# Performance work log

Measured on AMD Instinct MI355X. Metric: run time of the kernel, lower is better.

The kernel has to match this reference:

```python
import jax, jax.numpy as jnp
import numpy as np

N, E = 50000, 800000
IN, HID, OUT = 128, 128, 64
BN_EPS = 1e-5


def setup_inputs() -> dict:
    key = jax.random.key(0)
    ks = jax.random.split(key, 12)
    def glorot(k, shape):
        lim = float(np.sqrt(6.0 / (shape[0] + shape[1])))
        return jax.random.uniform(k, shape, jnp.float32, -lim, lim)
    return {
        "x": jax.random.normal(ks[0], (N, IN), jnp.float32),
        "edge_index": jax.random.randint(ks[1], (2, E), 0, N, jnp.int64),
        "W1": glorot(ks[2], (IN, HID)),  "b1": jnp.zeros((HID,), jnp.float32),
        "W2": glorot(ks[3], (HID, HID)), "b2": jnp.zeros((HID,), jnp.float32),
        "W3": glorot(ks[4], (HID, OUT)), "b3": jnp.zeros((OUT,), jnp.float32),
        "gamma1": jax.random.uniform(ks[5], (HID,), jnp.float32, 0.5, 1.5),
        "beta1": jax.random.normal(ks[6], (HID,), jnp.float32) * 0.1,
        "gamma2": jax.random.uniform(ks[7], (HID,), jnp.float32, 0.5, 1.5),
        "beta2": jax.random.normal(ks[8], (HID,), jnp.float32) * 0.1,
    }


def reference(x, edge_index, W1, b1, W2, b2, W3, b3, gamma1, beta1, gamma2, beta2):
    n = x.shape[0]
    loop = jnp.arange(n, dtype=edge_index.dtype)
    src = jnp.concatenate([edge_index[0], loop])  # add self-loops (PyG GCNConv)
    dst = jnp.concatenate([edge_index[1], loop])
    deg = jax.ops.segment_sum(jnp.ones_like(dst, dtype=x.dtype), dst, num_segments=n)
    dinv = jnp.where(deg > 0, deg ** -0.5, 0.0)
    norm = (dinv[src] * dinv[dst])[:, None]  # symmetric normalization per edge

    def conv(h, W, b):
        h = h @ W                                   # [N, out]
        agg = jax.ops.segment_sum(h[src] * norm, dst, num_segments=n)
        return agg + b

    def bn(h, g, b):  # training-mode BatchNorm1d (batch stats, biased var)
        m = h.mean(axis=0)
        v = h.var(axis=0)
        return (h - m) * jax.lax.rsqrt(v + BN_EPS) * g + b

    # layer 1: in==hidden so residual applies; dropout is a no-op in eval mode
    h = jax.nn.relu(bn(conv(x, W1, b1), gamma1, beta1))
    if h.shape == x.shape:
        h = h + x
    x = h
    # layer 2: hidden -> hidden, residual
    h = jax.nn.relu(bn(conv(x, W2, b2), gamma2, beta2))
    h = h + x
    x = h
    # output layer
    return conv(x, W3, b3)
```

## Files before the change

### kernel.cpp

```cpp
#include <hip/hip_runtime.h>


#define BN_EPS 1e-5f

typedef __attribute__((ext_vector_type(8))) short bf16x8;
typedef __attribute__((ext_vector_type(4))) float f32x4;

__device__ __forceinline__ float bf2f(unsigned short u) {
    unsigned v = ((unsigned)u) << 16;
    return __builtin_bit_cast(float, v);
}
__device__ __forceinline__ unsigned short f2bf(float f) {
    unsigned u = __builtin_bit_cast(unsigned, f);
    u += 0x7fffu + ((u >> 16) & 1u);
    return (unsigned short)(u >> 16);
}

__global__ __launch_bounds__(256) void k_hist_coarse(const int* __restrict__ dst,
                                                     int* __restrict__ ccnt, int e) {
    __shared__ int hist[256];
    const int t = threadIdx.x;
    hist[t] = 0;
    __syncthreads();
    const int base = blockIdx.x * 4096;
    const int end = min(base + 4096, e);
    for (int idx = base + t; idx < end; idx += 256)
        atomicAdd(&hist[dst[idx] >> 8], 1);
    __syncthreads();
    if (hist[t] > 0) atomicAdd(&ccnt[t], hist[t]);
}

__global__ void k_scan_coarse(const int* __restrict__ ccnt, int* __restrict__ cbase,
                              int* __restrict__ ccur) {
    __shared__ int buf[256];
    const int t = threadIdx.x;
    const int v = ccnt[t];
    buf[t] = v;
    __syncthreads();
    for (int off = 1; off < 256; off <<= 1) {
        int add = (t >= off) ? buf[t - off] : 0;
        __syncthreads();
        buf[t] += add;
        __syncthreads();
    }
    const int ex = buf[t] - v;
    cbase[t] = ex;
    ccur[t] = ex;
    if (t == 255) cbase[256] = buf[255];
}

__global__ __launch_bounds__(256) void k_partition(const int* __restrict__ src,
                                                   const int* __restrict__ dst,
                                                   int* __restrict__ ccur,
                                                   unsigned int* __restrict__ pairs, int e) {
    __shared__ unsigned short dl[4096], sl[4096];
    __shared__ int hist[256], basel[256], rnk[256];
    const int t = threadIdx.x;
    const int base = blockIdx.x * 4096;
    hist[t] = 0; rnk[t] = 0;
    __syncthreads();
#pragma unroll
    for (int i = 0; i < 16; ++i) {
        int idx = base + t + i * 256;
        if (idx < e) {
            int d = dst[idx];
            dl[t + i * 256] = (unsigned short)d;
            sl[t + i * 256] = (unsigned short)src[idx];
            atomicAdd(&hist[d >> 8], 1);
        }
    }
    __syncthreads();
    if (hist[t] > 0) basel[t] = atomicAdd(&ccur[t], hist[t]);
    __syncthreads();
#pragma unroll
    for (int i = 0; i < 16; ++i) {
        int idx = base + t + i * 256;
        if (idx < e) {
            int d = dl[t + i * 256];
            int bb = d >> 8;
            int r = atomicAdd(&rnk[bb], 1);
            pairs[basel[bb] + r] = (unsigned)d | ((unsigned)sl[t + i * 256] << 16);
        }
    }
}

__global__ __launch_bounds__(256) void k_fine(const unsigned int* __restrict__ pairs,
                                              const int* __restrict__ cbase,
                                              int* __restrict__ rs, int* __restrict__ eb,
                                              float* __restrict__ dinv, int n, int e) {
    __shared__ int hist[256], fbase[256], cur[256], tmp[256];
    const int t = threadIdx.x;
    const int b = blockIdx.x;
    const int lo = cbase[b], hi = cbase[b + 1];
    hist[t] = 0; cur[t] = 0;
    __syncthreads();
    for (int pos = lo + t; pos < hi; pos += 256)
        atomicAdd(&hist[pairs[pos] & 255], 1);
    __syncthreads();
    const int v = hist[t];
    tmp[t] = v;
    __syncthreads();
    for (int off = 1; off < 256; off <<= 1) {
        int add = (t >= off) ? tmp[t - off] : 0;
        __syncthreads();
        tmp[t] += add;
        __syncthreads();
    }
    fbase[t] = tmp[t] - v;
    __syncthreads();
    const int node = b * 256 + t;
    if (node < n) {
        rs[node] = lo + fbase[t];
        dinv[node] = rsqrtf((float)(hist[t] + 1));
    }
    if (b == 0 && t == 0) rs[n] = e;
    for (int pos = lo + t; pos < hi; pos += 256) {
        unsigned pr = pairs[pos];
        int local = pr & 255;
        int r = atomicAdd(&cur[local], 1);
        eb[lo + fbase[local] + r] = (int)(pr >> 16);
    }
}

__global__ void k_packW(const float* __restrict__ W, unsigned short* __restrict__ Wp, int ncol) {
    const int nct = ncol >> 4;
    int tid = blockIdx.x * 256 + threadIdx.x;
    if (tid >= 4 * nct * 64) return;
    int lane = tid & 63;
    int f = tid >> 6;
    int ct = f % nct;
    int kc = f / nct;
    int n = ct * 16 + (lane & 15);
    int k0 = kc * 32 + (lane >> 4) * 8;
    ushort4 lo, hi;
    lo.x = f2bf(W[(size_t)(k0 + 0) * ncol + n]);
    lo.y = f2bf(W[(size_t)(k0 + 1) * ncol + n]);
    lo.z = f2bf(W[(size_t)(k0 + 2) * ncol + n]);
    lo.w = f2bf(W[(size_t)(k0 + 3) * ncol + n]);
    hi.x = f2bf(W[(size_t)(k0 + 4) * ncol + n]);
    hi.y = f2bf(W[(size_t)(k0 + 5) * ncol + n]);
    hi.z = f2bf(W[(size_t)(k0 + 6) * ncol + n]);
    hi.w = f2bf(W[(size_t)(k0 + 7) * ncol + n]);
    *(ushort4*)(Wp + (size_t)tid * 8)     = lo;
    *(ushort4*)(Wp + (size_t)tid * 8 + 4) = hi;
}

__global__ __launch_bounds__(256) void k_gemm_mfma128(
        const unsigned short* __restrict__ Ab, const unsigned short* __restrict__ Wp,
        unsigned short* __restrict__ xs, const float* __restrict__ dinv, int n) {
    __shared__ __align__(16) unsigned short Wl[16384];
    const int t = threadIdx.x;
    {
        const ushort4* s = (const ushort4*)Wp;
        ushort4* d = (ushort4*)Wl;
#pragma unroll
        for (int i = 0; i < 16; ++i) d[t + 256 * i] = s[t + 256 * i];
    }
    __syncthreads();
    const int lane = t & 63, wave = t >> 6;
    const int quad = lane >> 4, l15 = lane & 15;
    const int m0 = blockIdx.x * 64 + wave * 16;
    const int arow = min(m0 + l15, n - 1);

    f32x4 acc[8];
#pragma unroll
    for (int ct = 0; ct < 8; ++ct) acc[ct] = (f32x4){0.f, 0.f, 0.f, 0.f};

#pragma unroll
    for (int kc = 0; kc < 4; ++kc) {
        bf16x8 a = *(const bf16x8*)(Ab + (size_t)arow * 128 + kc * 32 + quad * 8);
#pragma unroll
        for (int ct = 0; ct < 8; ++ct) {
            bf16x8 b = *(const bf16x8*)(Wl + ((kc * 8 + ct) * 64 + lane) * 8);
            acc[ct] = __builtin_amdgcn_mfma_f32_16x16x32_bf16(a, b, acc[ct], 0, 0, 0);
        }
    }

    int rowv[4]; float dvv[4];
#pragma unroll
    for (int r = 0; r < 4; ++r) {
        rowv[r] = m0 + quad * 4 + r;
        dvv[r] = dinv[min(rowv[r], n - 1)];
    }
#pragma unroll
    for (int ct = 0; ct < 8; ++ct)
#pragma unroll
        for (int r = 0; r < 4; ++r)
            if (rowv[r] < n)
                xs[(size_t)rowv[r] * 128 + ct * 16 + l15] = f2bf(acc[ct][r] * dvv[r]);
}

__global__ __launch_bounds__(256) void k_gemm_mfma128_f32(
        const float* __restrict__ Af, const unsigned short* __restrict__ Wp,
        unsigned short* __restrict__ xs, const float* __restrict__ dinv, int n) {
    __shared__ __align__(16) unsigned short Wl[16384];
    const int t = threadIdx.x;
    {
        const ushort4* s = (const ushort4*)Wp;
        ushort4* d = (ushort4*)Wl;
#pragma unroll
        for (int i = 0; i < 16; ++i) d[t + 256 * i] = s[t + 256 * i];
    }
    __syncthreads();
    const int lane = t & 63, wave = t >> 6;
    const int quad = lane >> 4, l15 = lane & 15;
    const int m0 = blockIdx.x * 64 + wave * 16;
    const int arow = min(m0 + l15, n - 1);

    f32x4 acc[8];
#pragma unroll
    for (int ct = 0; ct < 8; ++ct) acc[ct] = (f32x4){0.f, 0.f, 0.f, 0.f};

#pragma unroll
    for (int kc = 0; kc < 4; ++kc) {
        float4 alo = *(const float4*)(Af + (size_t)arow * 128 + kc * 32 + quad * 8);
        float4 ahi = *(const float4*)(Af + (size_t)arow * 128 + kc * 32 + quad * 8 + 4);
        bf16x8 a;
        a[0] = (short)f2bf(alo.x); a[1] = (short)f2bf(alo.y);
        a[2] = (short)f2bf(alo.z); a[3] = (short)f2bf(alo.w);
        a[4] = (short)f2bf(ahi.x); a[5] = (short)f2bf(ahi.y);
        a[6] = (short)f2bf(ahi.z); a[7] = (short)f2bf(ahi.w);
#pragma unroll
        for (int ct = 0; ct < 8; ++ct) {
            bf16x8 b = *(const bf16x8*)(Wl + ((kc * 8 + ct) * 64 + lane) * 8);
            acc[ct] = __builtin_amdgcn_mfma_f32_16x16x32_bf16(a, b, acc[ct], 0, 0, 0);
        }
    }

    int rowv[4]; float dvv[4];
#pragma unroll
    for (int r = 0; r < 4; ++r) {
        rowv[r] = m0 + quad * 4 + r;
        dvv[r] = dinv[min(rowv[r], n - 1)];
    }
#pragma unroll
    for (int ct = 0; ct < 8; ++ct)
#pragma unroll
        for (int r = 0; r < 4; ++r)
            if (rowv[r] < n)
                xs[(size_t)rowv[r] * 128 + ct * 16 + l15] = f2bf(acc[ct][r] * dvv[r]);
}

__global__ __launch_bounds__(256) void k_gemm_mfma64(
        const unsigned short* __restrict__ Ab, const unsigned short* __restrict__ Wp,
        unsigned short* __restrict__ xs, const float* __restrict__ dinv, int n) {
    __shared__ __align__(16) unsigned short Wl[8192];
    const int t = threadIdx.x;
    {
        const ushort4* s = (const ushort4*)Wp;
        ushort4* d = (ushort4*)Wl;
#pragma unroll
        for (int i = 0; i < 8; ++i) d[t + 256 * i] = s[t + 256 * i];
    }
    __syncthreads();
    const int lane = t & 63, wave = t >> 6;
    const int quad = lane >> 4, l15 = lane & 15;
    const int m0 = blockIdx.x * 64 + wave * 16;
    const int arow = min(m0 + l15, n - 1);

    f32x4 acc[4];
#pragma unroll
    for (int ct = 0; ct < 4; ++ct) acc[ct] = (f32x4){0.f, 0.f, 0.f, 0.f};

#pragma unroll
    for (int kc = 0; kc < 4; ++kc) {
        bf16x8 a = *(const bf16x8*)(Ab + (size_t)arow * 128 + kc * 32 + quad * 8);
#pragma unroll
        for (int ct = 0; ct < 4; ++ct) {
            bf16x8 b = *(const bf16x8*)(Wl + ((kc * 4 + ct) * 64 + lane) * 8);
            acc[ct] = __builtin_amdgcn_mfma_f32_16x16x32_bf16(a, b, acc[ct], 0, 0, 0);
        }
    }

    int rowv[4]; float dvv[4];
#pragma unroll
    for (int r = 0; r < 4; ++r) {
        rowv[r] = m0 + quad * 4 + r;
        dvv[r] = dinv[min(rowv[r], n - 1)];
    }
#pragma unroll
    for (int ct = 0; ct < 4; ++ct)
#pragma unroll
        for (int r = 0; r < 4; ++r)
            if (rowv[r] < n)
                xs[(size_t)rowv[r] * 64 + ct * 16 + l15] = f2bf(acc[ct][r] * dvv[r]);
}

__global__ void k_gather128(float* __restrict__ agg, const unsigned short* __restrict__ xs,
                            const int* __restrict__ rs, const int* __restrict__ eb,
                            const float* __restrict__ dinv, int n) {
    int node = blockIdx.x * 8 + (threadIdx.x >> 5);
    int lane = threadIdx.x & 31;
    if (node >= n) return;
    const ushort4* xv = (const ushort4*)xs;
    ushort4 v = xv[(size_t)node * 32 + lane];
    float ax0 = bf2f(v.x), ay0 = bf2f(v.y), az0 = bf2f(v.z), aw0 = bf2f(v.w);
    float ax1 = 0.f, ay1 = 0.f, az1 = 0.f, aw1 = 0.f;
    int b = rs[node], e = rs[node + 1];
    int i = b;
    for (; i + 2 <= e; i += 2) {
        int s0 = eb[i], s1 = eb[i + 1];
        ushort4 u0 = xv[(size_t)s0 * 32 + lane];
        ushort4 u1 = xv[(size_t)s1 * 32 + lane];
        ax0 += bf2f(u0.x); ay0 += bf2f(u0.y); az0 += bf2f(u0.z); aw0 += bf2f(u0.w);
        ax1 += bf2f(u1.x); ay1 += bf2f(u1.y); az1 += bf2f(u1.z); aw1 += bf2f(u1.w);
    }
    if (i < e) {
        ushort4 u = xv[(size_t)eb[i] * 32 + lane];
        ax0 += bf2f(u.x); ay0 += bf2f(u.y); az0 += bf2f(u.z); aw0 += bf2f(u.w);
    }
    float dv = dinv[node];
    float4 o;
    o.x = (ax0 + ax1) * dv; o.y = (ay0 + ay1) * dv;
    o.z = (az0 + az1) * dv; o.w = (aw0 + aw1) * dv;
    ((float4*)agg)[(size_t)node * 32 + lane] = o;
}

__global__ void k_gather64_bias(float* __restrict__ out, const unsigned short* __restrict__ xs,
                                const int* __restrict__ rs, const int* __restrict__ eb,
                                const float* __restrict__ dinv, const float* __restrict__ bias,
                                int n) {
    int node = blockIdx.x * 16 + (threadIdx.x >> 4);
    int lane = threadIdx.x & 15;
    if (node >= n) return;
    const ushort4* xv = (const ushort4*)xs;
    ushort4 v = xv[(size_t)node * 16 + lane];
    float ax0 = bf2f(v.x), ay0 = bf2f(v.y), az0 = bf2f(v.z), aw0 = bf2f(v.w);
    float ax1 = 0.f, ay1 = 0.f, az1 = 0.f, aw1 = 0.f;
    int b = rs[node], e = rs[node + 1];
    int i = b;
    for (; i + 2 <= e; i += 2) {
        int s0 = eb[i], s1 = eb[i + 1];
        ushort4 u0 = xv[(size_t)s0 * 16 + lane];
        ushort4 u1 = xv[(size_t)s1 * 16 + lane];
        ax0 += bf2f(u0.x); ay0 += bf2f(u0.y); az0 += bf2f(u0.z); aw0 += bf2f(u0.w);
        ax1 += bf2f(u1.x); ay1 += bf2f(u1.y); az1 += bf2f(u1.z); aw1 += bf2f(u1.w);
    }
    if (i < e) {
        ushort4 u = xv[(size_t)eb[i] * 16 + lane];
        ax0 += bf2f(u.x); ay0 += bf2f(u.y); az0 += bf2f(u.z); aw0 += bf2f(u.w);
    }
    float dv = dinv[node];
    const float4* bv = (const float4*)bias;
    float4 bb = bv[lane];
    float4 o;
    o.x = (ax0 + ax1) * dv + bb.x; o.y = (ay0 + ay1) * dv + bb.y;
    o.z = (az0 + az1) * dv + bb.z; o.w = (aw0 + aw1) * dv + bb.w;
    ((float4*)out)[(size_t)node * 16 + lane] = o;
}

__global__ void k_stats(const float* __restrict__ h, float* __restrict__ gsum,
                        float* __restrict__ gsq, int n) {
    int c = threadIdx.x & 127;
    int half = threadIdx.x >> 7;
    float s = 0.f, s2 = 0.f;
    for (int r = blockIdx.x * 2 + half; r < n; r += gridDim.x * 2) {
        float v = h[(size_t)r * 128 + c];
        s += v; s2 += v * v;
    }
    __shared__ float ls[256], ls2[256];
    ls[threadIdx.x] = s; ls2[threadIdx.x] = s2;
    __syncthreads();
    if (threadIdx.x < 128) {
        atomicAdd(&gsum[c], ls[threadIdx.x] + ls[threadIdx.x + 128]);
        atomicAdd(&gsq[c],  ls2[threadIdx.x] + ls2[threadIdx.x + 128]);
    }
}

__global__ void k_finalize(const float* __restrict__ gsum, const float* __restrict__ gsq,
                           const float* __restrict__ gamma, const float* __restrict__ beta,
                           float* __restrict__ scale, float* __restrict__ shift, float inv_n) {
    int c = threadIdx.x;
    float m = gsum[c] * inv_n;
    float v = gsq[c] * inv_n - m * m;
    float sc = gamma[c] * rsqrtf(v + BN_EPS);
    scale[c] = sc;
    shift[c] = beta[c] - m * sc;
}

__global__ void k_bnrelu_dual(float* __restrict__ h, unsigned short* __restrict__ hb,
                              const float* __restrict__ agg, const float* __restrict__ res,
                              const float* __restrict__ scale, const float* __restrict__ shift,
                              int total4) {
    int i = blockIdx.x * 256 + threadIdx.x;
    if (i >= total4) return;
    int c = (i * 4) & 127;
    float4 g  = ((const float4*)agg)[i];
    float4 rr = ((const float4*)res)[i];
    float4 sc = *(const float4*)(scale + c);
    float4 sh = *(const float4*)(shift + c);
    float4 o;
    o.x = fmaxf(fmaf(g.x, sc.x, sh.x), 0.f) + rr.x;
    o.y = fmaxf(fmaf(g.y, sc.y, sh.y), 0.f) + rr.y;
    o.z = fmaxf(fmaf(g.z, sc.z, sh.z), 0.f) + rr.z;
    o.w = fmaxf(fmaf(g.w, sc.w, sh.w), 0.f) + rr.w;
    ((float4*)h)[i] = o;
    ushort4 ob = { f2bf(o.x), f2bf(o.y), f2bf(o.z), f2bf(o.w) };
    ((ushort4*)hb)[i] = ob;
}

__global__ void k_bnrelu_bf(unsigned short* __restrict__ hb,
                            const float* __restrict__ agg, const float* __restrict__ res,
                            const float* __restrict__ scale, const float* __restrict__ shift,
                            int total4) {
    int i = blockIdx.x * 256 + threadIdx.x;
    if (i >= total4) return;
    int c = (i * 4) & 127;
    float4 g  = ((const float4*)agg)[i];
    float4 rr = ((const float4*)res)[i];
    float4 sc = *(const float4*)(scale + c);
    float4 sh = *(const float4*)(shift + c);
    ushort4 ob;
    ob.x = f2bf(fmaxf(fmaf(g.x, sc.x, sh.x), 0.f) + rr.x);
    ob.y = f2bf(fmaxf(fmaf(g.y, sc.y, sh.y), 0.f) + rr.y);
    ob.z = f2bf(fmaxf(fmaf(g.z, sc.z, sh.z), 0.f) + rr.z);
    ob.w = f2bf(fmaxf(fmaf(g.w, sc.w, sh.w), 0.f) + rr.w);
    ((ushort4*)hb)[i] = ob;
}

extern "C" void kernel_launch(void* const* d_in, const int* in_sizes, int n_in,
                              void* d_out, int out_size, void* d_ws, size_t ws_size,
                              hipStream_t stream) {
    const float* x   = (const float*)d_in[0];
    const int*   ei  = (const int*)d_in[1];
    const float* W1  = (const float*)d_in[2];
    const float* W2  = (const float*)d_in[4];
    const float* W3  = (const float*)d_in[6];
    const float* b3  = (const float*)d_in[7];
    const float* g1  = (const float*)d_in[8];
    const float* be1 = (const float*)d_in[9];
    const float* g2  = (const float*)d_in[10];
    const float* be2 = (const float*)d_in[11];
    float* out = (float*)d_out;

    const int N = in_sizes[0] / 128;
    const int E = in_sizes[1] / 2;
    const int* src = ei;
    const int* dst = ei + E;

    char* p = (char*)d_ws;
    float* dinv  = (float*)p;               p += (size_t)N * 4;
    unsigned short* xb = (unsigned short*)p; p += (size_t)N * 128 * 2;
    unsigned short* xs = (unsigned short*)p; p += (size_t)N * 128 * 2;
    float* agg   = (float*)p;               p += (size_t)N * 128 * 4;
    float* h1    = (float*)p;               p += (size_t)N * 128 * 4;
    float* gsum  = (float*)p;               p += 128 * 4;
    float* gsq   = (float*)p;               p += 128 * 4;
    float* scale = (float*)p;               p += 128 * 4;
    float* shift = (float*)p;               p += 128 * 4;
    unsigned short* Wp1 = (unsigned short*)p; p += 16384 * 2;
    unsigned short* Wp2 = (unsigned short*)p; p += 16384 * 2;
    unsigned short* Wp3 = (unsigned short*)p; p += 8192 * 2;
    int*   ccnt  = (int*)p;                 p += 256 * 4;
    int*   cbase = (int*)p;                 p += 260 * 4;
    int*   ccur  = (int*)p;                 p += 256 * 4;
    unsigned int* pairs = (unsigned int*)p; p += (size_t)E * 4;
    int*   rs    = (int*)p;                 p += (size_t)(N + 16) * 4;
    int*   eb    = (int*)p;                 p += (size_t)E * 4;

    const int B = 256;
    const int gT    = (N + 63) / 64;
    const int g4    = (N * 128 / 4 + B - 1) / B;
    const int gEchk = (E + 4095) / 4096;
    const int gN256 = (N + 255) / 256;
    const float inv_n = 1.0f / (float)N;

    hipMemsetAsync(ccnt, 0, 256 * 4, stream);
    k_hist_coarse<<<gEchk, B, 0, stream>>>(dst, ccnt, E);
    k_scan_coarse<<<1, B, 0, stream>>>(ccnt, cbase, ccur);
    k_partition<<<gEchk, B, 0, stream>>>(src, dst, ccur, pairs, E);
    k_fine<<<gN256, B, 0, stream>>>(pairs, cbase, rs, eb, dinv, N, E);
    k_packW<<<8, B, 0, stream>>>(W1, Wp1, 128);
    k_packW<<<8, B, 0, stream>>>(W2, Wp2, 128);
    k_packW<<<4, B, 0, stream>>>(W3, Wp3, 64);

    k_gemm_mfma128_f32<<<gT, B, 0, stream>>>(x, Wp1, xs, dinv, N);
    k_gather128<<<(N + 7) / 8, B, 0, stream>>>(agg, xs, rs, eb, dinv, N);
    hipMemsetAsync(gsum, 0, 2 * 128 * 4, stream);
    k_stats<<<512, B, 0, stream>>>(agg, gsum, gsq, N);
    k_finalize<<<1, 128, 0, stream>>>(gsum, gsq, g1, be1, scale, shift, inv_n);

    k_bnrelu_dual<<<g4, B, 0, stream>>>(h1, xb, agg, x, scale, shift, N * 128 / 4);
    k_gemm_mfma128<<<gT, B, 0, stream>>>(xb, Wp2, xs, dinv, N);
    k_gather128<<<(N + 7) / 8, B, 0, stream>>>(agg, xs, rs, eb, dinv, N);
    hipMemsetAsync(gsum, 0, 2 * 128 * 4, stream);
    k_stats<<<512, B, 0, stream>>>(agg, gsum, gsq, N);
    k_finalize<<<1, 128, 0, stream>>>(gsum, gsq, g2, be2, scale, shift, inv_n);

    k_bnrelu_bf<<<g4, B, 0, stream>>>(xb, agg, h1, scale, shift, N * 128 / 4);
    k_gemm_mfma64<<<gT, B, 0, stream>>>(xb, Wp3, xs, dinv, N);
    k_gather64_bias<<<(N + 15) / 16, B, 0, stream>>>(out, xs, rs, eb, dinv, b3, N);
}
```

Measured before the change: 353.8 us.

## Fuse BN stats into gather and BN/ReLU/residual into following GEMM

The BatchNorm statistics reduction now happens inside a grid-stride gather kernel that accumulates per-thread sums and writes them with atomics, so the separate stats pass over agg goes away. The BN+ReLU+residual elementwise kernels are folded into the A-operand load of the next MFMA GEMM, which removes the intermediate bf16 buffer round trip. The gather loops are also unrolled by 4 for more memory-level parallelism. The cost is extra register pressure and a fixed 1024-block grid for the gather, which may lower occupancy.

```diff
diff --git a/kernel.cpp b/kernel.cpp
--- a/kernel.cpp
+++ b/kernel.cpp
@@ -145,51 +145,6 @@
     *(ushort4*)(Wp + (size_t)tid * 8 + 4) = hi;
 }
 
-__global__ __launch_bounds__(256) void k_gemm_mfma128(
-        const unsigned short* __restrict__ Ab, const unsigned short* __restrict__ Wp,
-        unsigned short* __restrict__ xs, const float* __restrict__ dinv, int n) {
-    __shared__ __align__(16) unsigned short Wl[16384];
-    const int t = threadIdx.x;
-    {
-        const ushort4* s = (const ushort4*)Wp;
-        ushort4* d = (ushort4*)Wl;
-#pragma unroll
-        for (int i = 0; i < 16; ++i) d[t + 256 * i] = s[t + 256 * i];
-    }
-    __syncthreads();
-    const int lane = t & 63, wave = t >> 6;
-    const int quad = lane >> 4, l15 = lane & 15;
-    const int m0 = blockIdx.x * 64 + wave * 16;
-    const int arow = min(m0 + l15, n - 1);
-
-    f32x4 acc[8];
-#pragma unroll
-    for (int ct = 0; ct < 8; ++ct) acc[ct] = (f32x4){0.f, 0.f, 0.f, 0.f};
-
-#pragma unroll
-    for (int kc = 0; kc < 4; ++kc) {
-        bf16x8 a = *(const bf16x8*)(Ab + (size_t)arow * 128 + kc * 32 + quad * 8);
-#pragma unroll
-        for (int ct = 0; ct < 8; ++ct) {
-            bf16x8 b = *(const bf16x8*)(Wl + ((kc * 8 + ct) * 64 + lane) * 8);
-            acc[ct] = __builtin_amdgcn_mfma_f32_16x16x32_bf16(a, b, acc[ct], 0, 0, 0);
-        }
-    }
-
-    int rowv[4]; float dvv[4];
-#pragma unroll
-    for (int r = 0; r < 4; ++r) {
-        rowv[r] = m0 + quad * 4 + r;
-        dvv[r] = dinv[min(rowv[r], n - 1)];
-    }
-#pragma unroll
-    for (int ct = 0; ct < 8; ++ct)
-#pragma unroll
-        for (int r = 0; r < 4; ++r)
-            if (rowv[r] < n)
-                xs[(size_t)rowv[r] * 128 + ct * 16 + l15] = f2bf(acc[ct][r] * dvv[r]);
-}
-
 __global__ __launch_bounds__(256) void k_gemm_mfma128_f32(
         const float* __restrict__ Af, const unsigned short* __restrict__ Wp,
         unsigned short* __restrict__ xs, const float* __restrict__ dinv, int n) {
@@ -241,30 +196,118 @@
                 xs[(size_t)rowv[r] * 128 + ct * 16 + l15] = f2bf(acc[ct][r] * dvv[r]);
 }
 
-__global__ __launch_bounds__(256) void k_gemm_mfma64(
-        const unsigned short* __restrict__ Ab, const unsigned short* __restrict__ Wp,
+__global__ __launch_bounds__(256) void k_gemm_mfma128_bn(
+        const float* __restrict__ agg, const float* __restrict__ res,
+        const float* __restrict__ scale, const float* __restrict__ shift,
+        float* __restrict__ h_out, const unsigned short* __restrict__ Wp,
         unsigned short* __restrict__ xs, const float* __restrict__ dinv, int n) {
-    __shared__ __align__(16) unsigned short Wl[8192];
+    __shared__ __align__(16) unsigned short Wl[16384];
+    __shared__ float s_sc[128], s_sh[128];
     const int t = threadIdx.x;
     {
         const ushort4* s = (const ushort4*)Wp;
         ushort4* d = (ushort4*)Wl;
 #pragma unroll
-        for (int i = 0; i < 8; ++i) d[t + 256 * i] = s[t + 256 * i];
-    }
+        for (int i = 0; i < 16; ++i) d[t + 256 * i] = s[t + 256 * i];
+    }
+    if (t < 128) s_sc[t] = scale[t];
+    else         s_sh[t - 128] = shift[t - 128];
     __syncthreads();
     const int lane = t & 63, wave = t >> 6;
     const int quad = lane >> 4, l15 = lane & 15;
     const int m0 = blockIdx.x * 64 + wave * 16;
     const int arow = min(m0 + l15, n - 1);
 
+    f32x4 acc[8];
+#pragma unroll
+    for (int ct = 0; ct < 8; ++ct) acc[ct] = (f32x4){0.f, 0.f, 0.f, 0.f};
+
+#pragma unroll
+    for (int kc = 0; kc < 4; ++kc) {
+        const int f = kc * 32 + quad * 8;
+        float4 g0 = *(const float4*)(agg + (size_t)arow * 128 + f);
+        float4 g1 = *(const float4*)(agg + (size_t)arow * 128 + f + 4);
+        float4 r0 = *(const float4*)(res + (size_t)arow * 128 + f);
+        float4 r1 = *(const float4*)(res + (size_t)arow * 128 + f + 4);
+        float4 h0, h1;
+        h0.x = fmaxf(fmaf(g0.x, s_sc[f + 0], s_sh[f + 0]), 0.f) + r0.x;
+        h0.y = fmaxf(fmaf(g0.y, s_sc[f + 1], s_sh[f + 1]), 0.f) + r0.y;
+        h0.z = fmaxf(fmaf(g0.z, s_sc[f + 2], s_sh[f + 2]), 0.f) + r0.z;
+        h0.w = fmaxf(fmaf(g0.w, s_sc[f + 3], s_sh[f + 3]), 0.f) + r0.w;
+        h1.x = fmaxf(fmaf(g1.x, s_sc[f + 4], s_sh[f + 4]), 0.f) + r1.x;
+        h1.y = fmaxf(fmaf(g1.y, s_sc[f + 5], s_sh[f + 5]), 0.f) + r1.y;
+        h1.z = fmaxf(fmaf(g1.z, s_sc[f + 6], s_sh[f + 6]), 0.f) + r1.z;
+        h1.w = fmaxf(fmaf(g1.w, s_sc[f + 7], s_sh[f + 7]), 0.f) + r1.w;
+        *(float4*)(h_out + (size_t)arow * 128 + f)     = h0;
+        *(float4*)(h_out + (size_t)arow * 128 + f + 4) = h1;
+        bf16x8 a;
+        a[0] = (short)f2bf(h0.x); a[1] = (short)f2bf(h0.y);
+        a[2] = (short)f2bf(h0.z); a[3] = (short)f2bf(h0.w);
+        a[4] = (short)f2bf(h1.x); a[5] = (short)f2bf(h1.y);
+        a[6] = (short)f2bf(h1.z); a[7] = (short)f2bf(h1.w);
+#pragma unroll
+        for (int ct = 0; ct < 8; ++ct) {
+            bf16x8 b = *(const bf16x8*)(Wl + ((kc * 8 + ct) * 64 + lane) * 8);
+            acc[ct] = __builtin_amdgcn_mfma_f32_16x16x32_bf16(a, b, acc[ct], 0, 0, 0);
+        }
+    }
+
+    int rowv[4]; float dvv[4];
+#pragma unroll
+    for (int r = 0; r < 4; ++r) {
+        rowv[r] = m0 + quad * 4 + r;
+        dvv[r] = dinv[min(rowv[r], n - 1)];
+    }
+#pragma unroll
+    for (int ct = 0; ct < 8; ++ct)
+#pragma unroll
+        for (int r = 0; r < 4; ++r)
+            if (rowv[r] < n)
+                xs[(size_t)rowv[r] * 128 + ct * 16 + l15] = f2bf(acc[ct][r] * dvv[r]);
+}
+
+__global__ __launch_bounds__(256) void k_gemm_mfma64_bn(
+        const float* __restrict__ agg, const float* __restrict__ res,
+        const float* __restrict__ scale, const float* __restrict__ shift,
+        const unsigned short* __restrict__ Wp,
+        unsigned short* __restrict__ xs, const float* __restrict__ dinv, int n) {
+    __shared__ __align__(16) unsigned short Wl[8192];
+    __shared__ float s_sc[128], s_sh[128];
+    const int t = threadIdx.x;
+    {
+        const ushort4* s = (const ushort4*)Wp;
+        ushort4* d = (ushort4*)Wl;
+#pragma unroll
+        for (int i = 0; i < 8; ++i) d[t + 256 * i] = s[t + 256 * i];
+    }
+    if (t < 128) s_sc[t] = scale[t];
+    else         s_sh[t - 128] = shift[t - 128];
+    __syncthreads();
+    const int lane = t & 63, wave = t >> 6;
+    const int quad = lane >> 4, l15 = lane & 15;
+    const int m0 = blockIdx.x * 64 + wave * 16;
+    const int arow = min(m0 + l15, n - 1);
+
     f32x4 acc[4];
 #pragma unroll
     for (int ct = 0; ct < 4; ++ct) acc[ct] = (f32x4){0.f, 0.f, 0.f, 0.f};
 
 #pragma unroll
     for (int kc = 0; kc < 4; ++kc) {
-        bf16x8 a = *(const bf16x8*)(Ab + (size_t)arow * 128 + kc * 32 + quad * 8);
+        const int f = kc * 32 + quad * 8;
+        float4 g0 = *(const float4*)(agg + (size_t)arow * 128 + f);
+        float4 g1 = *(const float4*)(agg + (size_t)arow * 128 + f + 4);
+        float4 r0 = *(const float4*)(res + (size_t)arow * 128 + f);
+        float4 r1 = *(const float4*)(res + (size_t)arow * 128 + f + 4);
+        bf16x8 a;
+        a[0] = (short)f2bf(fmaxf(fmaf(g0.x, s_sc[f + 0], s_sh[f + 0]), 0.f) + r0.x);
+        a[1] = (short)f2bf(fmaxf(fmaf(g0.y, s_sc[f + 1], s_sh[f + 1]), 0.f) + r0.y);
+        a[2] = (short)f2bf(fmaxf(fmaf(g0.z, s_sc[f + 2], s_sh[f + 2]), 0.f) + r0.z);
+        a[3] = (short)f2bf(fmaxf(fmaf(g0.w, s_sc[f + 3], s_sh[f + 3]), 0.f) + r0.w);
+        a[4] = (short)f2bf(fmaxf(fmaf(g1.x, s_sc[f + 4], s_sh[f + 4]), 0.f) + r1.x);
+        a[5] = (short)f2bf(fmaxf(fmaf(g1.y, s_sc[f + 5], s_sh[f + 5]), 0.f) + r1.y);
+        a[6] = (short)f2bf(fmaxf(fmaf(g1.z, s_sc[f + 6], s_sh[f + 6]), 0.f) + r1.z);
+        a[7] = (short)f2bf(fmaxf(fmaf(g1.w, s_sc[f + 7], s_sh[f + 7]), 0.f) + r1.w);
 #pragma unroll
         for (int ct = 0; ct < 4; ++ct) {
             bf16x8 b = *(const bf16x8*)(Wl + ((kc * 4 + ct) * 64 + lane) * 8);
@@ -286,34 +329,65 @@
                 xs[(size_t)rowv[r] * 64 + ct * 16 + l15] = f2bf(acc[ct][r] * dvv[r]);
 }
 
-__global__ void k_gather128(float* __restrict__ agg, const unsigned short* __restrict__ xs,
-                            const int* __restrict__ rs, const int* __restrict__ eb,
-                            const float* __restrict__ dinv, int n) {
-    int node = blockIdx.x * 8 + (threadIdx.x >> 5);
-    int lane = threadIdx.x & 31;
-    if (node >= n) return;
+__global__ __launch_bounds__(256) void k_gather128_stats(
+        float* __restrict__ agg, const unsigned short* __restrict__ xs,
+        const int* __restrict__ rs, const int* __restrict__ eb,
+        const float* __restrict__ dinv, float* __restrict__ gsum,
+        float* __restrict__ gsq, int n) {
+    const int t = threadIdx.x;
+    const int lane = t & 31;
+    const int slot = t >> 5;
     const ushort4* xv = (const ushort4*)xs;
-    ushort4 v = xv[(size_t)node * 32 + lane];
-    float ax0 = bf2f(v.x), ay0 = bf2f(v.y), az0 = bf2f(v.z), aw0 = bf2f(v.w);
-    float ax1 = 0.f, ay1 = 0.f, az1 = 0.f, aw1 = 0.f;
-    int b = rs[node], e = rs[node + 1];
-    int i = b;
-    for (; i + 2 <= e; i += 2) {
-        int s0 = eb[i], s1 = eb[i + 1];
-        ushort4 u0 = xv[(size_t)s0 * 32 + lane];
-        ushort4 u1 = xv[(size_t)s1 * 32 + lane];
-        ax0 += bf2f(u0.x); ay0 += bf2f(u0.y); az0 += bf2f(u0.z); aw0 += bf2f(u0.w);
-        ax1 += bf2f(u1.x); ay1 += bf2f(u1.y); az1 += bf2f(u1.z); aw1 += bf2f(u1.w);
-    }
-    if (i < e) {
-        ushort4 u = xv[(size_t)eb[i] * 32 + lane];
-        ax0 += bf2f(u.x); ay0 += bf2f(u.y); az0 += bf2f(u.z); aw0 += bf2f(u.w);
-    }
-    float dv = dinv[node];
-    float4 o;
-    o.x = (ax0 + ax1) * dv; o.y = (ay0 + ay1) * dv;
-    o.z = (az0 + az1) * dv; o.w = (aw0 + aw1) * dv;
-    ((float4*)agg)[(size_t)node * 32 + lane] = o;
+    float sx = 0.f, sy = 0.f, sz = 0.f, sw = 0.f;
+    float qx = 0.f, qy = 0.f, qz = 0.f, qw = 0.f;
+
+    for (int node = blockIdx.x * 8 + slot; node < n; node += gridDim.x * 8) {
+        ushort4 v = xv[(size_t)node * 32 + lane];
+        float ax0 = bf2f(v.x), ay0 = bf2f(v.y), az0 = bf2f(v.z), aw0 = bf2f(v.w);
+        float ax1 = 0.f, ay1 = 0.f, az1 = 0.f, aw1 = 0.f;
+        int b = rs[node], e = rs[node + 1];
+        int i = b;
+        for (; i + 4 <= e; i += 4) {
+            int sA = eb[i], sB = eb[i + 1], sC = eb[i + 2], sD = eb[i + 3];
+            ushort4 uA = xv[(size_t)sA * 32 + lane];
+            ushort4 uB = xv[(size_t)sB * 32 + lane];
+            ushort4 uC = xv[(size_t)sC * 32 + lane];
+            ushort4 uD = xv[(size_t)sD * 32 + lane];
+            ax0 += bf2f(uA.x); ay0 += bf2f(uA.y); az0 += bf2f(uA.z); aw0 += bf2f(uA.w);
+            ax1 += bf2f(uB.x); ay1 += bf2f(uB.y); az1 += bf2f(uB.z); aw1 += bf2f(uB.w);
+            ax0 += bf2f(uC.x); ay0 += bf2f(uC.y); az0 += bf2f(uC.z); aw0 += bf2f(uC.w);
+            ax1 += bf2f(uD.x); ay1 += bf2f(uD.y); az1 += bf2f(uD.z); aw1 += bf2f(uD.w);
+        }
+        for (; i < e; ++i) {
+            ushort4 u = xv[(size_t)eb[i] * 32 + lane];
+            ax0 += bf2f(u.x); ay0 += bf2f(u.y); az0 += bf2f(u.z); aw0 += bf2f(u.w);
+        }
+        float dv = dinv[node];
+        float4 o;
+        o.x = (ax0 + ax1) * dv; o.y = (ay0 + ay1) * dv;
+        o.z = (az0 + az1) * dv; o.w = (aw0 + aw1) * dv;
+        ((float4*)agg)[(size_t)node * 32 + lane] = o;
+        sx += o.x; sy += o.y; sz += o.z; sw += o.w;
+        qx += o.x * o.x; qy += o.y * o.y; qz += o.z * o.z; qw += o.w * o.w;
+    }
+
+    __shared__ float4 lsum[256], lsq[256];
+    lsum[t] = (float4){sx, sy, sz, sw};
+    lsq[t]  = (float4){qx, qy, qz, qw};
+    __syncthreads();
+    if (t < 32) {
+        float4 a = lsum[t], b = lsq[t];
+#pragma unroll
+        for (int g = 1; g < 8; ++g) {
+            float4 u = lsum[t + 32 * g], w = lsq[t + 32 * g];
+            a.x += u.x; a.y += u.y; a.z += u.z; a.w += u.w;
+            b.x += w.x; b.y += w.y; b.z += w.z; b.w += w.w;
+        }
+        atomicAdd(&gsum[4 * t + 0], a.x); atomicAdd(&gsum[4 * t + 1], a.y);
+        atomicAdd(&gsum[4 * t + 2], a.z); atomicAdd(&gsum[4 * t + 3], a.w);
+        atomicAdd(&gsq[4 * t + 0], b.x);  atomicAdd(&gsq[4 * t + 1], b.y);
+        atomicAdd(&gsq[4 * t + 2], b.z);  atomicAdd(&gsq[4 * t + 3], b.w);
+    }
 }
 
 __global__ void k_gather64_bias(float* __restrict__ out, const unsigned short* __restrict__ xs,
@@ -329,14 +403,18 @@
     float ax1 = 0.f, ay1 = 0.f, az1 = 0.f, aw1 = 0.f;
     int b = rs[node], e = rs[node + 1];
     int i = b;
-    for (; i + 2 <= e; i += 2) {
-        int s0 = eb[i], s1 = eb[i + 1];
-        ushort4 u0 = xv[(size_t)s0 * 16 + lane];
-        ushort4 u1 = xv[(size_t)s1 * 16 + lane];
-        ax0 += bf2f(u0.x); ay0 += bf2f(u0.y); az0 += bf2f(u0.z); aw0 += bf2f(u0.w);
-        ax1 += bf2f(u1.x); ay1 += bf2f(u1.y); az1 += bf2f(u1.z); aw1 += bf2f(u1.w);
-    }
-    if (i < e) {
+    for (; i + 4 <= e; i += 4) {
+        int sA = eb[i], sB = eb[i + 1], sC = eb[i + 2], sD = eb[i + 3];
+        ushort4 uA = xv[(size_t)sA * 16 + lane];
+        ushort4 uB = xv[(size_t)sB * 16 + lane];
+        ushort4 uC = xv[(size_t)sC * 16 + lane];
+        ushort4 uD = xv[(size_t)sD * 16 + lane];
+        ax0 += bf2f(uA.x); ay0 += bf2f(uA.y); az0 += bf2f(uA.z); aw0 += bf2f(uA.w);
+        ax1 += bf2f(uB.x); ay1 += bf2f(uB.y); az1 += bf2f(uB.z); aw1 += bf2f(uB.w);
+        ax0 += bf2f(uC.x); ay0 += bf2f(uC.y); az0 += bf2f(uC.z); aw0 += bf2f(uC.w);
+        ax1 += bf2f(uD.x); ay1 += bf2f(uD.y); az1 += bf2f(uD.z); aw1 += bf2f(uD.w);
+    }
+    for (; i < e; ++i) {
         ushort4 u = xv[(size_t)eb[i] * 16 + lane];
         ax0 += bf2f(u.x); ay0 += bf2f(u.y); az0 += bf2f(u.z); aw0 += bf2f(u.w);
     }
@@ -347,24 +425,6 @@
     o.x = (ax0 + ax1) * dv + bb.x; o.y = (ay0 + ay1) * dv + bb.y;
     o.z = (az0 + az1) * dv + bb.z; o.w = (aw0 + aw1) * dv + bb.w;
     ((float4*)out)[(size_t)node * 16 + lane] = o;
-}
-
-__global__ void k_stats(const float* __restrict__ h, float* __restrict__ gsum,
-                        float* __restrict__ gsq, int n) {
-    int c = threadIdx.x & 127;
-    int half = threadIdx.x >> 7;
-    float s = 0.f, s2 = 0.f;
-    for (int r = blockIdx.x * 2 + half; r < n; r += gridDim.x * 2) {
-        float v = h[(size_t)r * 128 + c];
-        s += v; s2 += v * v;
-    }
-    __shared__ float ls[256], ls2[256];
-    ls[threadIdx.x] = s; ls2[threadIdx.x] = s2;
-    __syncthreads();
-    if (threadIdx.x < 128) {
-        atomicAdd(&gsum[c], ls[threadIdx.x] + ls[threadIdx.x + 128]);
-        atomicAdd(&gsq[c],  ls2[threadIdx.x] + ls2[threadIdx.x + 128]);
-    }
 }
 
 __global__ void k_finalize(const float* __restrict__ gsum, const float* __restrict__ gsq,
@@ -376,46 +436,6 @@
     float sc = gamma[c] * rsqrtf(v + BN_EPS);
     scale[c] = sc;
     shift[c] = beta[c] - m * sc;
-}
-
-__global__ void k_bnrelu_dual(float* __restrict__ h, unsigned short* __restrict__ hb,
-                              const float* __restrict__ agg, const float* __restrict__ res,
-                              const float* __restrict__ scale, const float* __restrict__ shift,
-                              int total4) {
-    int i = blockIdx.x * 256 + threadIdx.x;
-    if (i >= total4) return;
-    int c = (i * 4) & 127;
-    float4 g  = ((const float4*)agg)[i];
-    float4 rr = ((const float4*)res)[i];
-    float4 sc = *(const float4*)(scale + c);
-    float4 sh = *(const float4*)(shift + c);
-    float4 o;
-    o.x = fmaxf(fmaf(g.x, sc.x, sh.x), 0.f) + rr.x;
-    o.y = fmaxf(fmaf(g.y, sc.y, sh.y), 0.f) + rr.y;
-    o.z = fmaxf(fmaf(g.z, sc.z, sh.z), 0.f) + rr.z;
-    o.w = fmaxf(fmaf(g.w, sc.w, sh.w), 0.f) + rr.w;
-    ((float4*)h)[i] = o;
-    ushort4 ob = { f2bf(o.x), f2bf(o.y), f2bf(o.z), f2bf(o.w) };
-    ((ushort4*)hb)[i] = ob;
-}
-
-__global__ void k_bnrelu_bf(unsigned short* __restrict__ hb,
-                            const float* __restrict__ agg, const float* __restrict__ res,
-                            const float* __restrict__ scale, const float* __restrict__ shift,
-                            int total4) {
-    int i = blockIdx.x * 256 + threadIdx.x;
-    if (i >= total4) return;
-    int c = (i * 4) & 127;
-    float4 g  = ((const float4*)agg)[i];
-    float4 rr = ((const float4*)res)[i];
-    float4 sc = *(const float4*)(scale + c);
-    float4 sh = *(const float4*)(shift + c);
-    ushort4 ob;
-    ob.x = f2bf(fmaxf(fmaf(g.x, sc.x, sh.x), 0.f) + rr.x);
-    ob.y = f2bf(fmaxf(fmaf(g.y, sc.y, sh.y), 0.f) + rr.y);
-    ob.z = f2bf(fmaxf(fmaf(g.z, sc.z, sh.z), 0.f) + rr.z);
-    ob.w = f2bf(fmaxf(fmaf(g.w, sc.w, sh.w), 0.f) + rr.w);
-    ((ushort4*)hb)[i] = ob;
 }
 
 extern "C" void kernel_launch(void* const* d_in, const int* in_sizes, int n_in,
@@ -440,7 +460,6 @@
 
     char* p = (char*)d_ws;
     float* dinv  = (float*)p;               p += (size_t)N * 4;
-    unsigned short* xb = (unsigned short*)p; p += (size_t)N * 128 * 2;
     unsigned short* xs = (unsigned short*)p; p += (size_t)N * 128 * 2;
     float* agg   = (float*)p;               p += (size_t)N * 128 * 4;
     float* h1    = (float*)p;               p += (size_t)N * 128 * 4;
@@ -460,9 +479,9 @@
 
     const int B = 256;
     const int gT    = (N + 63) / 64;
-    const int g4    = (N * 128 / 4 + B - 1) / B;
     const int gEchk = (E + 4095) / 4096;
     const int gN256 = (N + 255) / 256;
+    const int gG    = 1024;
     const float inv_n = 1.0f / (float)N;
 
     hipMemsetAsync(ccnt, 0, 256 * 4, stream);
@@ -475,19 +494,15 @@
     k_packW<<<4, B, 0, stream>>>(W3, Wp3, 64);
 
     k_gemm_mfma128_f32<<<gT, B, 0, stream>>>(x, Wp1, xs, dinv, N);
-    k_gather128<<<(N + 7) / 8, B, 0, stream>>>(agg, xs, rs, eb, dinv, N);
     hipMemsetAsync(gsum, 0, 2 * 128 * 4, stream);
-    k_stats<<<512, B, 0, stream>>>(agg, gsum, gsq, N);
+    k_gather128_stats<<<gG, B, 0, stream>>>(agg, xs, rs, eb, dinv, gsum, gsq, N);
     k_finalize<<<1, 128, 0, stream>>>(gsum, gsq, g1, be1, scale, shift, inv_n);
 
-    k_bnrelu_dual<<<g4, B, 0, stream>>>(h1, xb, agg, x, scale, shift, N * 128 / 4);
-    k_gemm_mfma128<<<gT, B, 0, stream>>>(xb, Wp2, xs, dinv, N);
-    k_gather128<<<(N + 7) / 8, B, 0, stream>>>(agg, xs, rs, eb, dinv, N);
+    k_gemm_mfma128_bn<<<gT, B, 0, stream>>>(agg, x, scale, shift, h1, Wp2, xs, dinv, N);
     hipMemsetAsync(gsum, 0, 2 * 128 * 4, stream);
-    k_stats<<<512, B, 0, stream>>>(agg, gsum, gsq, N);
+    k_gather128_stats<<<gG, B, 0, stream>>>(agg, xs, rs, eb, dinv, gsum, gsq, N);
     k_finalize<<<1, 128, 0, stream>>>(gsum, gsq, g2, be2, scale, shift, inv_n);
 
-    k_bnrelu_bf<<<g4, B, 0, stream>>>(xb, agg, h1, scale, shift, N * 128 / 4);
-    k_gemm_mfma64<<<gT, B, 0, stream>>>(xb, Wp3, xs, dinv, N);
+    k_gemm_mfma64_bn<<<gT, B, 0, stream>>>(agg, h1, scale, shift, Wp3, xs, dinv, N);
     k_gather64_bias<<<(N + 15) / 16, B, 0, stream>>>(out, xs, rs, eb, dinv, b3, N);
 }
```

Result: slower. 486.5 us (+37.5%).
